# Optimization experiments

Hardware: AMD Instinct MI355X
Metric: run time of the kernel (lower is better)

Reference implementation:

```python
import jax, jax.numpy as jnp
import numpy as np

CTX_LEN = 7
TAU = 2.0      # curr_temp = max_temp at init
ALPHA = -1.0   # dist_to_logits_alpha


def _prelu(v, a):
    return jnp.where(v >= 0, v, a * v)


def setup_inputs() -> dict:
    key = jax.random.key(0)
    ks = jax.random.split(key, 8)
    B, T, D, M = 8, 4096, 256, 1024
    x = jax.random.normal(ks[0], (B, T, D), dtype=jnp.float32)
    noise = jax.random.normal(ks[1], (B, D, T - 1 + CTX_LEN), dtype=jnp.float32)
    gumbel_u = jax.random.uniform(ks[2], (B * T, M), dtype=jnp.float32)
    embedding = jax.random.uniform(ks[3], (1, M, D), dtype=jnp.float32)  # nn.init.uniform_
    w_ctx = jax.random.normal(ks[4], (D, D, CTX_LEN), dtype=jnp.float32) * 0.02
    w_f1 = jax.random.normal(ks[5], (D, 2 * D), dtype=jnp.float32) * 0.04
    w_f2 = jax.random.normal(ks[6], (D, 2 * D), dtype=jnp.float32) * 0.04
    a1 = jnp.array(0.5, dtype=jnp.float32)
    a2 = jnp.array(0.5, dtype=jnp.float32)
    return {"x": x, "noise": noise, "gumbel_u": gumbel_u, "epo": 10,
            "embedding": embedding, "w_ctx": w_ctx, "w_f1": w_f1, "a1": a1,
            "w_f2": w_f2, "a2": a2}


def reference(x, noise, gumbel_u, epo, embedding, w_ctx, w_f1, a1, w_f2, a2):
    B, T, D = x.shape
    E = embedding[0]                      # [M, D]
    M = E.shape[0]
    xt = jnp.transpose(x, (0, 2, 1))      # [B, D, T]
    # context input: x[:, :-1] permuted, left-padded by 1+7-1=7, detached
    ctx_in = jax.lax.stop_gradient(jnp.pad(xt[:, :, :T - 1], ((0, 0), (0, 0), (CTX_LEN, 0))))
    scale = jnp.sqrt(jnp.mean(ctx_in ** 2, axis=(1, 2), keepdims=True))
    ctx_in_noisy = jax.lax.stop_gradient(ctx_in + 0.5 * scale * noise * (0.5 ** (epo / 10.0)))
    ctx_out = jax.lax.conv_general_dilated(
        ctx_in_noisy, w_ctx, (1,), 'VALID',
        dimension_numbers=('NCH', 'OIH', 'NCH'))   # [B, D, T]
    # fuse 1 (1x1 conv == channel matmul) + PReLU
    cat1 = jnp.concatenate([xt, ctx_out], axis=1)            # [B, 2D, T]
    cur = _prelu(jnp.einsum('oc,bct->bot', w_f1, cat1), a1)  # [B, D, T]
    cur = jnp.transpose(cur, (0, 2, 1)).reshape(-1, D)       # [B*T, D]
    # squared distances via addmm equivalent, scaled to logits
    dist = (jnp.sum(cur ** 2, axis=1, keepdims=True)
            + jnp.sum(E ** 2, axis=1)
            - 2.0 * cur @ E.T)                               # [B*T, M]
    dm = ALPHA * dist
    # hard code usage entropy
    k = jnp.argmax(dm, axis=-1)
    hard_probs = jnp.mean(jax.nn.one_hot(k, M, dtype=dm.dtype), axis=0)
    code_perplexity = -jnp.sum(hard_probs * jnp.log2(hard_probs + 1e-10))
    # soft usage entropy
    avg_probs = jnp.mean(jax.nn.softmax(dm, axis=-1), axis=0)
    prob_perplexity = -jnp.sum(avg_probs * jnp.log2(avg_probs + 1e-10))
    # hard gumbel-softmax (straight-through)
    u = jnp.clip(gumbel_u, 1e-10, 1.0 - 1e-7)
    g = -jnp.log(-jnp.log(u))
    y_soft = jax.nn.softmax((dm + g) / TAU, axis=-1)
    idx = jnp.argmax(y_soft, axis=-1)
    y_hard = jax.nn.one_hot(idx, M, dtype=y_soft.dtype)
    dm_st = y_hard - jax.lax.stop_gradient(y_soft) + y_soft  # [B*T, M]
    quantization_inds = idx.reshape(B, T, 1)
    # dequantize: one-hot (straight-through) times codebook
    out_q = (dm_st @ E).reshape(B, T, D)
    # fuse 2 + PReLU
    cat2 = jnp.concatenate([jnp.transpose(out_q, (0, 2, 1)), ctx_out], axis=1)
    quantized = jnp.transpose(_prelu(jnp.einsum('oc,bct->bot', w_f2, cat2), a2), (0, 2, 1))
    return quantized, code_perplexity, prob_perplexity, quantization_inds
```

## Files before the change

### kernel.cpp

```cpp
#include <hip/hip_runtime.h>
#include <cmath>

#define B_    8
#define T_    4096
#define D_    256
#define M_    1024
#define L_    4102
#define LP_   4104
#define CTX_  7
#define NROW_ 32768

constexpr size_t OFF_DM    = 0;
constexpr size_t OFF_XT    = 0;
constexpr size_t OFF_CTXN  = 33554432;
constexpr size_t OFF_CURT  = 33554432;
constexpr size_t OFF_CTXO  = OFF_CTXN + (size_t)B_ * D_ * LP_;
constexpr size_t OFF_CUR2  = OFF_CTXO + (size_t)B_ * D_ * T_;
constexpr size_t OFF_SOFT  = OFF_CUR2 + NROW_;
constexpr size_t OFF_HIST  = OFF_SOFT + 4096;
constexpr size_t OFF_SUMSQ = OFF_HIST + 1024;
constexpr size_t OFF_ESQ   = OFF_SUMSQ + 16;
constexpr size_t OFF_IDX   = OFF_ESQ + 1024;
constexpr size_t OFF_ET    = OFF_IDX + NROW_;
constexpr size_t OFF_W1T   = OFF_ET + 262144;
constexpr size_t OFF_W2T   = OFF_W1T + 131072;
constexpr size_t OFF_WCT   = OFF_W2T + 131072;
constexpr size_t OFF_P     = OFF_WCT + 458752;

using s16x8 = __attribute__((ext_vector_type(8))) short;
using f32x4 = __attribute__((ext_vector_type(4))) float;

__device__ __forceinline__ ushort bf16rne(float f) {
  uint u = __float_as_uint(f);
  u += 0x7fffu + ((u >> 16) & 1u);
  return (ushort)(u >> 16);
}
__device__ __forceinline__ float bf16tof(ushort h) {
  return __uint_as_float((uint)h << 16);
}

__global__ __launch_bounds__(256) void k_prep(const float* __restrict__ emb,
                                              const float* __restrict__ wf1,
                                              const float* __restrict__ wf2,
                                              const float* __restrict__ wctx,
                                              const float* __restrict__ x,
                                              float* __restrict__ ET,
                                              float* __restrict__ W1T,
                                              float* __restrict__ W2T,
                                              ushort* __restrict__ WPF,
                                              float* __restrict__ esq,
                                              float* __restrict__ sumsq) {
  const int id = blockIdx.x;
  if (id < 512) {
    __shared__ float tile[32][33];
    const int tx = threadIdx.x & 31, ty = threadIdx.x >> 5;
    const float* src; float* dst; int R, C, c0, r0;
    if (id < 256)      { src = emb;  dst = ET;  R = 1024; C = 256;  c0 = (id & 7) << 5;  r0 = (id >> 3) << 5; }
    else if (id < 384) { const int r = id - 256; src = wf1; dst = W1T; R = 256; C = 512; c0 = (r & 15) << 5; r0 = (r >> 4) << 5; }
    else               { const int r = id - 384; src = wf2; dst = W2T; R = 256; C = 512; c0 = (r & 15) << 5; r0 = (r >> 4) << 5; }
    for (int rr = ty; rr < 32; rr += 8) {
      const int rI = r0 + rr, cI = c0 + tx;
      tile[rr][tx] = (rI < R && cI < C) ? src[(size_t)rI * C + cI] : 0.f;
    }
    __syncthreads();
    for (int rr = ty; rr < 32; rr += 8) {
      const int cI = c0 + rr, rI = r0 + tx;
      if (cI < C && rI < R) dst[(size_t)cI * R + rI] = tile[tx][rr];
    }
  } else if (id < 736) {
    const int K8 = id - 512;
    const int h = K8 >> 5, j = K8 & 31;
    const int o = threadIdx.x;
    uint hp[4], lp[4];
    #pragma unroll
    for (int e2 = 0; e2 < 4; ++e2) {
      ushort hs[2], ls[2];
      #pragma unroll
      for (int k = 0; k < 2; ++k) {
        const int i = (j << 3) + (e2 << 1) + k;
        const float v = wctx[(size_t)o * 1792 + (size_t)i * 7 + h];
        const ushort hb = bf16rne(v);
        hs[k] = hb;
        ls[k] = bf16rne(v - bf16tof(hb));
      }
      hp[e2] = (uint)hs[0] | ((uint)hs[1] << 16);
      lp[e2] = (uint)ls[0] | ((uint)ls[1] << 16);
    }
    uint4* W = (uint4*)WPF;
    W[(size_t)(K8 * 2) * 256 + o]     = make_uint4(hp[0], hp[1], hp[2], hp[3]);
    W[(size_t)(K8 * 2 + 1) * 256 + o] = make_uint4(lp[0], lp[1], lp[2], lp[3]);
  } else if (id < 992) {
    const int row = ((id - 736) << 2) + (threadIdx.x >> 6);
    const int lane = threadIdx.x & 63;
    const float4 v = ((const float4*)emb)[((size_t)row << 6) + lane];
    float s = v.x * v.x + v.y * v.y + v.z * v.z + v.w * v.w;
    #pragma unroll
    for (int off = 32; off; off >>= 1) s += __shfl_down(s, off, 64);
    if (lane == 0) esq[row] = s;
  } else {
    const int chunk = id - 992;
    const int b = chunk >> 6, sub = chunk & 63;
    const float4* xb = (const float4*)(x + (size_t)b * T_ * D_);
    const int N4 = (T_ - 1) * D_ / 4;
    float s = 0.f;
    for (int j = sub * 256 + threadIdx.x; j < N4; j += 64 * 256) {
      float4 v = xb[j];
      s += v.x * v.x + v.y * v.y + v.z * v.z + v.w * v.w;
    }
    #pragma unroll
    for (int off = 32; off; off >>= 1) s += __shfl_down(s, off, 64);
    __shared__ float red[4];
    const int lane = threadIdx.x & 63, wv = threadIdx.x >> 6;
    if (lane == 0) red[wv] = s;
    __syncthreads();
    if (threadIdx.x == 0) atomicAdd(&sumsq[b], (red[0] + red[1]) + (red[2] + red[3]));
  }
}

__global__ __launch_bounds__(256) void k_noisy(const float* __restrict__ x,
                                               const float* __restrict__ noise,
                                               const int* __restrict__ epo,
                                               const float* __restrict__ sumsq,
                                               ushort* __restrict__ inT,
                                               float* __restrict__ xT) {
  const int b = blockIdx.z;
  const int i0 = blockIdx.y << 5;
  const int tau0 = blockIdx.x << 5;
  const int tx = threadIdx.x & 31, ty = threadIdx.x >> 5;
  __shared__ float xt[32][33];
  __shared__ float nz[32][33];
  const int tr0 = tau0 - CTX_;
  for (int r = ty; r < 32; r += 8) {
    const int t = tr0 + r;
    xt[r][tx] = (t >= 0 && t < T_) ? x[((size_t)b * T_ + t) * D_ + i0 + tx] : 0.f;
  }
  for (int r = ty; r < 32; r += 8) {
    const int tau = tau0 + tx;
    nz[r][tx] = (tau < L_) ? noise[((size_t)b * D_ + i0 + r) * L_ + tau] : 0.f;
  }
  __syncthreads();
  const float scale = sqrtf(sumsq[b] * (1.0f / (256.0f * 4102.0f)));
  const float coef = 0.5f * powf(0.5f, (float)epo[0] * 0.1f) * scale;
  for (int r = ty; r < 32; r += 8) {
    const int i = i0 + r;
    const int tau = tau0 + tx;
    const float xv = xt[tx][r];
    if (tau >= CTX_ && tau < T_ + CTX_)
      xT[((size_t)b * D_ + i) * T_ + (tau - CTX_)] = xv;
  }
  if (threadIdx.x < 128) {
    const int tau_r = threadIdx.x >> 2, jl = threadIdx.x & 3;
    const int tau = tau0 + tau_r;
    if (tau < L_) {
      uint hp[4], lp[4];
      #pragma unroll
      for (int e2 = 0; e2 < 4; ++e2) {
        ushort hs[2], ls[2];
        #pragma unroll
        for (int k = 0; k < 2; ++k) {
          const int ir = (jl << 3) + (e2 << 1) + k;
          const float v = coef * nz[ir][tau_r] + xt[tau_r][ir];
          const ushort hb = bf16rne(v);
          hs[k] = hb;
          ls[k] = bf16rne(v - bf16tof(hb));
        }
        hp[e2] = (uint)hs[0] | ((uint)hs[1] << 16);
        lp[e2] = (uint)ls[0] | ((uint)ls[1] << 16);
      }
      const int j = (i0 >> 3) + jl;
      const int jsw = j ^ (tau & 7);
      ushort* dst = inT + ((size_t)b * LP_ + tau) * 256 + (jsw << 3);
      *(uint4*)dst = make_uint4(hp[0], hp[1], hp[2], hp[3]);
      *(uint4*)(dst + (size_t)B_ * LP_ * 256) = make_uint4(lp[0], lp[1], lp[2], lp[3]);
    }
  }
}

__global__ __launch_bounds__(256, 2) void k_convm(const ushort* __restrict__ WPF,
                                                  const ushort* __restrict__ inT,
                                                  float* __restrict__ ctxo) {
  const int t0 = blockIdx.x << 6;
  const int b  = blockIdx.y;
  const int tid = threadIdx.x;
  const int lane = tid & 63;
  const int wv = tid >> 6;
  const int ln = lane & 15, lg = lane >> 4;
  __shared__ ushort sB[2 * 72 * 256];
  {
    const size_t rb = ((size_t)b * LP_ + t0) * 256;
    const uint4* s4h = (const uint4*)(inT + rb);
    const uint4* s4l = (const uint4*)(inT + (size_t)B_ * LP_ * 256 + rb);
    uint4* d4 = (uint4*)sB;
    for (int q = tid; q < 2304; q += 256) d4[q] = s4h[q];
    for (int q = tid; q < 2304; q += 256) d4[2304 + q] = s4l[q];
  }
  __syncthreads();

  const f32x4 fz = {0.f, 0.f, 0.f, 0.f};
  f32x4 acc[4][4];
  #pragma unroll
  for (int i = 0; i < 4; ++i)
    #pragma unroll
    for (int j = 0; j < 4; ++j) acc[i][j] = fz;

  const ushort* wp = WPF + ((size_t)lg * 512 + (wv << 6) + ln) * 8;

  #pragma unroll 1
  for (int h = 0; h < 7; ++h) {
    #pragma unroll 1
    for (int js = 0; js < 8; ++js) {
      const int K8b = (h << 5) + (js << 2);
      s16x8 Af[2][4];
      #pragma unroll
      for (int to = 0; to < 4; ++to) {
        const ushort* ap = wp + (size_t)(K8b * 512 + (to << 4)) * 8;
        Af[0][to] = *(const s16x8*)ap;
        Af[1][to] = *(const s16x8*)(ap + 2048);
      }
      s16x8 Bf[2][4];
      #pragma unroll
      for (int tt = 0; tt < 4; ++tt) {
        const int r = (tt << 4) + ln + h;
        const int jsw = ((js << 2) + lg) ^ (r & 7);
        const int e0 = r * 256 + (jsw << 3);
        Bf[0][tt] = *(const s16x8*)&sB[e0];
        Bf[1][tt] = *(const s16x8*)&sB[18432 + e0];
      }
      #pragma unroll
      for (int to = 0; to < 4; ++to)
        #pragma unroll
        for (int tt = 0; tt < 4; ++tt) {
          acc[to][tt] = __builtin_amdgcn_mfma_f32_16x16x32_bf16(Af[0][to], Bf[0][tt], acc[to][tt], 0, 0, 0);
          acc[to][tt] = __builtin_amdgcn_mfma_f32_16x16x32_bf16(Af[0][to], Bf[1][tt], acc[to][tt], 0, 0, 0);
          acc[to][tt] = __builtin_amdgcn_mfma_f32_16x16x32_bf16(Af[1][to], Bf[0][tt], acc[to][tt], 0, 0, 0);
        }
    }
  }
  float* cb = ctxo + ((size_t)b * 256 + (wv << 6)) * T_ + t0;
  #pragma unroll
  for (int to = 0; to < 4; ++to)
    #pragma unroll
    for (int tt = 0; tt < 4; ++tt)
      #pragma unroll
      for (int rg = 0; rg < 4; ++rg) {
        const int o_loc = (to << 4) + (lg << 2) + rg;
        cb[(size_t)o_loc * T_ + (tt << 4) + ln] = acc[to][tt][rg];
      }
}

__device__ __forceinline__ void stage16x128(float* __restrict__ dst,
                                            const float* __restrict__ src,
                                            const int gstride, const int tid) {
  #pragma unroll
  for (int p = 0; p < 2; ++p) {
    const int q = p * 256 + tid;
    const int r = q >> 5, c = (q & 31) << 2;
    *(float4*)&dst[(r << 7) + c] = *(const float4*)&src[(size_t)r * gstride + c];
  }
}

__device__ __forceinline__ void gemm16s(const float* __restrict__ sA,
                                        const float* __restrict__ sB,
                                        const int ay, const int bx4,
                                        float acc[8][8]) {
  #pragma unroll 4
  for (int c = 0; c < 16; ++c) {
    const float4 a0 = *(const float4*)&sA[(c << 7) + ay];
    const float4 a1 = *(const float4*)&sA[(c << 7) + ay + 4];
    const float4 b0 = *(const float4*)&sB[(c << 7) + bx4];
    const float4 b1 = *(const float4*)&sB[(c << 7) + bx4 + 64];
    const float av[8] = {a0.x, a0.y, a0.z, a0.w, a1.x, a1.y, a1.z, a1.w};
    const float bv[8] = {b0.x, b0.y, b0.z, b0.w, b1.x, b1.y, b1.z, b1.w};
    #pragma unroll
    for (int i = 0; i < 8; ++i)
      #pragma unroll
      for (int j = 0; j < 8; ++j)
        acc[i][j] = fmaf(av[i], bv[j], acc[i][j]);
  }
}

__global__ __launch_bounds__(256) void k_fuse1(const float* __restrict__ xT,
                                               const float* __restrict__ ctxo,
                                               const float* __restrict__ w1T,
                                               const float* __restrict__ a1,
                                               float* __restrict__ curT,
                                               float* __restrict__ cur2) {
  const int bk = blockIdx.x;
  const int b = bk >> 5;
  const int t0 = (bk & 31) << 7;
  const int o0 = blockIdx.y << 7;
  const int tid = threadIdx.x;
  const int tx = tid & 15, ty = tid >> 4;
  const int ox = ty << 3, tp4 = tx << 2;
  __shared__ float smem[4096];
  float* sW = smem;
  float* sX = smem + 2048;
  float acc[8][8] = {};
  for (int cc = 0; cc < 512; cc += 16) {
    __syncthreads();
    stage16x128(sW, w1T + (size_t)cc * 256 + o0, 256, tid);
    const float* xsrc = (cc < 256)
        ? xT + ((size_t)b * D_ + cc) * T_ + t0
        : ctxo + ((size_t)b * D_ + (cc - 256)) * T_ + t0;
    stage16x128(sX, xsrc, T_, tid);
    __syncthreads();
    gemm16s(sW, sX, ox, tp4, acc);
  }
  const float alpha = a1[0];
  const size_t row0 = (size_t)b * T_ + t0;
  float part[8] = {};
  #pragma unroll
  for (int oo = 0; oo < 8; ++oo) {
    #pragma unroll
    for (int j = 0; j < 8; ++j) {
      float v = acc[oo][j];
      v = (v >= 0.f) ? v : alpha * v;
      acc[oo][j] = v;
      part[j] = fmaf(v, v, part[j]);
    }
    const float4 v0 = {acc[oo][0], acc[oo][1], acc[oo][2], acc[oo][3]};
    const float4 v1 = {acc[oo][4], acc[oo][5], acc[oo][6], acc[oo][7]};
    float* dst = curT + (size_t)(o0 + ox + oo) * NROW_ + row0;
    *(float4*)(dst + tp4) = v0;
    *(float4*)(dst + tp4 + 64) = v1;
  }
  __syncthreads();
  float* red = smem;
  #pragma unroll
  for (int j = 0; j < 4; ++j) {
    red[(tp4 + j) * 17 + ty] = part[j];
    red[(tp4 + 64 + j) * 17 + ty] = part[4 + j];
  }
  __syncthreads();
  if (tid < 128) {
    float s = 0.f;
    #pragma unroll
    for (int k = 0; k < 16; ++k) s += red[tid * 17 + k];
    atomicAdd(&cur2[row0 + tid], s);
  }
}

__global__ __launch_bounds__(256) void k_pmm(const float* __restrict__ ET,
                                             const float* __restrict__ w2T,
                                             float* __restrict__ P) {
  const int m0 = blockIdx.x << 7;
  const int o0 = blockIdx.y << 7;
  const int tid = threadIdx.x;
  const int tx = tid & 15, ty = tid >> 4;
  const int my = ty << 3, ox4 = tx << 2;
  __shared__ float smem[4096];
  float* sM = smem;
  float* sW = smem + 2048;
  float acc[8][8] = {};
  for (int cc = 0; cc < 256; cc += 16) {
    __syncthreads();
    stage16x128(sM, ET + (size_t)cc * M_ + m0, M_, tid);
    stage16x128(sW, w2T + (size_t)cc * 256 + o0, 256, tid);
    __syncthreads();
    gemm16s(sM, sW, my, ox4, acc);
  }
  #pragma unroll
  for (int mm = 0; mm < 8; ++mm) {
    const float4 v0 = {acc[mm][0], acc[mm][1], acc[mm][2], acc[mm][3]};
    const float4 v1 = {acc[mm][4], acc[mm][5], acc[mm][6], acc[mm][7]};
    float* dst = P + (size_t)(m0 + my + mm) * 256 + o0;
    *(float4*)(dst + ox4) = v0;
    *(float4*)(dst + ox4 + 64) = v1;
  }
}

__global__ __launch_bounds__(256) void k_dist(const float* __restrict__ curT,
                                              const float* __restrict__ ET,
                                              const float* __restrict__ cur2,
                                              const float* __restrict__ esq,
                                              float* __restrict__ dm) {
  const int r0 = blockIdx.x << 7;
  const int m0 = blockIdx.y << 7;
  const int tid = threadIdx.x;
  const int tx = tid & 15, ty = tid >> 4;
  const int ry = ty << 3, mx4 = tx << 2;
  __shared__ float smem[4096];
  float* sC = smem;
  float* sE = smem + 2048;
  float acc[8][8] = {};
  for (int cc = 0; cc < 256; cc += 16) {
    __syncthreads();
    stage16x128(sC, curT + (size_t)cc * NROW_ + r0, NROW_, tid);
    stage16x128(sE, ET + (size_t)cc * M_ + m0, M_, tid);
    __syncthreads();
    gemm16s(sC, sE, ry, mx4, acc);
  }
  float c2[8], eq0[4], eq1[4];
  *(float4*)&c2[0] = *(const float4*)&cur2[r0 + ry];
  *(float4*)&c2[4] = *(const float4*)&cur2[r0 + ry + 4];
  *(float4*)&eq0[0] = *(const float4*)&esq[m0 + mx4];
  *(float4*)&eq1[0] = *(const float4*)&esq[m0 + mx4 + 64];
  #pragma unroll
  for (int rr = 0; rr < 8; ++rr) {
    float o0v[4], o1v[4];
    #pragma unroll
    for (int j = 0; j < 4; ++j) {
      o0v[j] = -(c2[rr] + eq0[j] - 2.0f * acc[rr][j]);
      o1v[j] = -(c2[rr] + eq1[j] - 2.0f * acc[rr][j + 4]);
    }
    float* dst = dm + (size_t)(r0 + ry + rr) * M_ + m0;
    *(float4*)(dst + mx4) = *(float4*)&o0v[0];
    *(float4*)(dst + mx4 + 64) = *(float4*)&o1v[0];
  }
}

__global__ __launch_bounds__(256) void k_soft(const float* __restrict__ dm,
                                              const float* __restrict__ gu,
                                              float* __restrict__ soft4,
                                              unsigned* __restrict__ hist,
                                              int* __restrict__ idxi,
                                              float* __restrict__ idxf) {
  const int tid = threadIdx.x;
  const int lane = tid & 63, w = tid >> 6;
  __shared__ float accS[1024];
  __shared__ unsigned histS[1024];
  for (int j = tid; j < 1024; j += 256) { accS[j] = 0.f; histS[j] = 0u; }
  __syncthreads();
  float p[16] = {};
  const int rbase = (blockIdx.x << 6) + (w << 4);
  for (int rr = 0; rr < 16; ++rr) {
    const int r = rbase + rr;
    const float4* dr = (const float4*)(dm + ((size_t)r << 10));
    float v[16];
    #pragma unroll
    for (int k = 0; k < 4; ++k) {
      const float4 d = dr[lane + (k << 6)];
      v[k * 4 + 0] = d.x; v[k * 4 + 1] = d.y; v[k * 4 + 2] = d.z; v[k * 4 + 3] = d.w;
    }
    float mx = v[0];
    #pragma unroll
    for (int s = 1; s < 16; ++s) mx = fmaxf(mx, v[s]);
    #pragma unroll
    for (int m = 32; m; m >>= 1) mx = fmaxf(mx, __shfl_xor(mx, m, 64));
    float e[16]; float sum = 0.f;
    #pragma unroll
    for (int s = 0; s < 16; ++s) { e[s] = expf(v[s] - mx); sum += e[s]; }
    #pragma unroll
    for (int m = 32; m; m >>= 1) sum += __shfl_xor(sum, m, 64);
    const float inv = 1.0f / sum;
    #pragma unroll
    for (int s = 0; s < 16; ++s) p[s] = fmaf(e[s], inv, p[s]);
    float bv = v[0]; int bi = (lane << 2);
    #pragma unroll
    for (int s = 1; s < 16; ++s) {
      const int m_ = (lane << 2) + ((s >> 2) << 8) + (s & 3);
      if (v[s] > bv) { bv = v[s]; bi = m_; }
    }
    #pragma unroll
    for (int m = 32; m; m >>= 1) {
      const float ov = __shfl_xor(bv, m, 64);
      const int oi = __shfl_xor(bi, m, 64);
      if (ov > bv || (ov == bv && oi < bi)) { bv = ov; bi = oi; }
    }
    if (lane == 0) atomicAdd(&histS[bi], 1u);
    const float4* gr = (const float4*)(gu + ((size_t)r << 10));
    float z[16];
    #pragma unroll
    for (int k = 0; k < 4; ++k) {
      const float4 u = gr[lane + (k << 6)];
      const float uu[4] = {u.x, u.y, u.z, u.w};
      #pragma unroll
      for (int j = 0; j < 4; ++j) {
        const float uc = fminf(fmaxf(uu[j], 1e-10f), 1.0f - 1e-7f);
        z[k * 4 + j] = v[k * 4 + j] - logf(-logf(uc));
      }
    }
    bv = z[0]; bi = (lane << 2);
    #pragma unroll
    for (int s = 1; s < 16; ++s) {
      const int m_ = (lane << 2) + ((s >> 2) << 8) + (s & 3);
      if (z[s] > bv) { bv = z[s]; bi = m_; }
    }
    #pragma unroll
    for (int m = 32; m; m >>= 1) {
      const float ov = __shfl_xor(bv, m, 64);
      const int oi = __shfl_xor(bi, m, 64);
      if (ov > bv || (ov == bv && oi < bi)) { bv = ov; bi = oi; }
    }
    if (lane == 0) { idxi[r] = bi; idxf[r] = (float)bi; }
  }
  #pragma unroll
  for (int s = 0; s < 16; ++s)
    atomicAdd(&accS[(lane << 2) + ((s >> 2) << 8) + (s & 3)], p[s]);
  __syncthreads();
  const int rep = (blockIdx.x & 3) << 10;
  for (int j = tid; j < 1024; j += 256) {
    atomicAdd(&soft4[rep + j], accS[j]);
    const unsigned h = histS[j];
    if (h) atomicAdd(&hist[j], h);
  }
}

__global__ __launch_bounds__(256) void k_perp(const float* __restrict__ soft4,
                                              const unsigned* __restrict__ hist,
                                              float* __restrict__ out2) {
  const int tid = threadIdx.x;
  float cp = 0.f, pp = 0.f;
  for (int m = tid; m < 1024; m += 256) {
    const float hp = (float)hist[m] * (1.0f / 32768.0f);
    cp += hp * log2f(hp + 1e-10f);
    const float q = (soft4[m] + soft4[1024 + m] + soft4[2048 + m] + soft4[3072 + m]) * (1.0f / 32768.0f);
    pp += q * log2f(q + 1e-10f);
  }
  #pragma unroll
  for (int off = 32; off; off >>= 1) {
    cp += __shfl_down(cp, off, 64);
    pp += __shfl_down(pp, off, 64);
  }
  __shared__ float rc[4], rp[4];
  const int lane = tid & 63, wv = tid >> 6;
  if (lane == 0) { rc[wv] = cp; rp[wv] = pp; }
  __syncthreads();
  if (tid == 0) {
    out2[0] = -((rc[0] + rc[1]) + (rc[2] + rc[3]));
    out2[1] = -((rp[0] + rp[1]) + (rp[2] + rp[3]));
  }
}

__global__ __launch_bounds__(256) void k_fuse2m(const float* __restrict__ ctxo,
                                                const float* __restrict__ w2T,
                                                const float* __restrict__ P,
                                                const int* __restrict__ idxi,
                                                const float* __restrict__ a2,
                                                float* __restrict__ outq) {
  const int bk = blockIdx.x;
  const int b = bk >> 6;
  const int t0 = (bk & 63) << 6;
  const int tid = threadIdx.x;
  const int lane = tid & 63, wv = tid >> 6;
  const int ln = lane & 15, lg = lane >> 4;
  const int o0w = wv << 6;
  __shared__ int idxS[64];
  if (tid < 64) idxS[tid] = idxi[(size_t)b * T_ + t0 + tid];
  __syncthreads();

  const f32x4 fz = {0.f, 0.f, 0.f, 0.f};
  f32x4 acc[4][4];
  #pragma unroll
  for (int i = 0; i < 4; ++i)
    #pragma unroll
    for (int j = 0; j < 4; ++j) acc[i][j] = fz;

  #pragma unroll 1
  for (int ks = 0; ks < 8; ++ks) {
    const int cb = (ks << 5) + (lg << 3);
    s16x8 Af[4];
    #pragma unroll
    for (int to = 0; to < 4; ++to) {
      const float* wp = w2T + (size_t)(256 + cb) * 256 + o0w + (to << 4) + ln;
      #pragma unroll
      for (int e = 0; e < 8; ++e)
        Af[to][e] = (short)bf16rne(wp[(size_t)e * 256]);
    }
    s16x8 Bf[4];
    #pragma unroll
    for (int tt = 0; tt < 4; ++tt) {
      const float* xp = ctxo + ((size_t)b * D_ + cb) * T_ + t0 + (tt << 4) + ln;
      #pragma unroll
      for (int e = 0; e < 8; ++e)
        Bf[tt][e] = (short)bf16rne(xp[(size_t)e * T_]);
    }
    #pragma unroll
    for (int to = 0; to < 4; ++to)
      #pragma unroll
      for (int tt = 0; tt < 4; ++tt)
        acc[to][tt] = __builtin_amdgcn_mfma_f32_16x16x32_bf16(Af[to], Bf[tt], acc[to][tt], 0, 0, 0);
  }

  const float alpha = a2[0];
  #pragma unroll
  for (int tt = 0; tt < 4; ++tt) {
    const int t = t0 + (tt << 4) + ln;
    const int id = idxS[(tt << 4) + ln];
    #pragma unroll
    for (int to = 0; to < 4; ++to) {
      const int ob = o0w + (to << 4) + (lg << 2);
      const float4 p4 = *(const float4*)&P[(size_t)id * 256 + ob];
      const float pv[4] = {p4.x, p4.y, p4.z, p4.w};
      float o[4];
      #pragma unroll
      for (int rg = 0; rg < 4; ++rg) {
        const float v = acc[to][tt][rg] + pv[rg];
        o[rg] = (v >= 0.f) ? v : alpha * v;
      }
      *(float4*)&outq[((size_t)b * T_ + t) * D_ + ob] = *(float4*)&o[0];
    }
  }
}

extern "C" void kernel_launch(void* const* d_in, const int* in_sizes, int n_in,
                              void* d_out, int out_size, void* d_ws, size_t ws_size,
                              hipStream_t stream) {
  (void)in_sizes; (void)n_in; (void)out_size; (void)ws_size;
  const float* x     = (const float*)d_in[0];
  const float* noise = (const float*)d_in[1];
  const float* gu    = (const float*)d_in[2];
  const int*   epo   = (const int*)d_in[3];
  const float* emb   = (const float*)d_in[4];
  const float* wctx  = (const float*)d_in[5];
  const float* wf1   = (const float*)d_in[6];
  const float* a1    = (const float*)d_in[7];
  const float* wf2   = (const float*)d_in[8];
  const float* a2    = (const float*)d_in[9];

  float* ws    = (float*)d_ws;
  float* dm    = ws + OFF_DM;
  float* xT    = ws + OFF_XT;
  ushort* inT  = (ushort*)(ws + OFF_CTXN);
  float* curT  = ws + OFF_CURT;
  float* ctxo  = ws + OFF_CTXO;
  float* cur2  = ws + OFF_CUR2;
  float* soft  = ws + OFF_SOFT;
  unsigned* hist = (unsigned*)(ws + OFF_HIST);
  float* sumsq = ws + OFF_SUMSQ;
  float* esq   = ws + OFF_ESQ;
  int*   idxi  = (int*)(ws + OFF_IDX);
  float* ET    = ws + OFF_ET;
  float* W1T   = ws + OFF_W1T;
  float* W2T   = ws + OFF_W2T;
  ushort* WPF  = (ushort*)(ws + OFF_WCT);
  float* P     = ws + OFF_P;

  float* outq = (float*)d_out;
  float* scal = outq + (size_t)NROW_ * D_;
  float* idxf = scal + 2;

  hipMemsetAsync(ws + OFF_CUR2, 0, (NROW_ + 4096 + 1024 + 16) * sizeof(float), stream);

  k_prep  <<<1504, 256, 0, stream>>>(emb, wf1, wf2, wctx, x, ET, W1T, W2T, WPF, esq, sumsq);
  k_noisy <<<dim3(129, 8, 8), 256, 0, stream>>>(x, noise, epo, sumsq, inT, xT);
  k_convm <<<dim3(64, 8), 256, 0, stream>>>(WPF, inT, ctxo);
  k_fuse1 <<<dim3(256, 2), 256, 0, stream>>>(xT, ctxo, W1T, a1, curT, cur2);
  k_pmm   <<<dim3(8, 2), 256, 0, stream>>>(ET, W2T, P);
  k_dist  <<<dim3(256, 8), 256, 0, stream>>>(curT, ET, cur2, esq, dm);
  k_soft  <<<512, 256, 0, stream>>>(dm, gu, soft, hist, idxi, idxf);
  k_perp  <<<1, 256, 0, stream>>>(soft, hist, scal);
  k_fuse2m<<<512, 256, 0, stream>>>(ctxo, W2T, P, idxi, a2, outq);
}
```

Measured before the change: 790.0 us.

## Fuse distance GEMM with softmax/argmax epilogue to skip dm round-trip

Merges the distance GEMM and the softmax/gumbel/argmax kernel into one kernel. Each block computes a full 32x1024 row tile of logits in registers and reduces it directly, so the 128 MB dm matrix is never written to or read from global memory. In exchange, each block now stages the entire codebook slice (64 KB shared) per k-step, uses a less efficient 8x16 per-thread GEMM shape with a large register footprint, and rereads ET 1024 times.

```diff
diff --git a/kernel.cpp b/kernel.cpp
--- a/kernel.cpp
+++ b/kernel.cpp
@@ -10,7 +10,6 @@
 #define CTX_  7
 #define NROW_ 32768
 
-constexpr size_t OFF_DM    = 0;
 constexpr size_t OFF_XT    = 0;
 constexpr size_t OFF_CTXN  = 33554432;
 constexpr size_t OFF_CURT  = 33554432;
@@ -369,69 +368,74 @@
   }
 }
 
-__global__ __launch_bounds__(256) void k_dist(const float* __restrict__ curT,
-                                              const float* __restrict__ ET,
-                                              const float* __restrict__ cur2,
-                                              const float* __restrict__ esq,
-                                              float* __restrict__ dm) {
-  const int r0 = blockIdx.x << 7;
-  const int m0 = blockIdx.y << 7;
+__global__ __launch_bounds__(256, 2) void k_dsoft(const float* __restrict__ curT,
+                                                  const float* __restrict__ ET,
+                                                  const float* __restrict__ cur2,
+                                                  const float* __restrict__ esq,
+                                                  const float* __restrict__ gu,
+                                                  float* __restrict__ soft4,
+                                                  unsigned* __restrict__ hist,
+                                                  int* __restrict__ idxi,
+                                                  float* __restrict__ idxf) {
   const int tid = threadIdx.x;
-  const int tx = tid & 15, ty = tid >> 4;
-  const int ry = ty << 3, mx4 = tx << 2;
-  __shared__ float smem[4096];
-  float* sC = smem;
-  float* sE = smem + 2048;
-  float acc[8][8] = {};
-  for (int cc = 0; cc < 256; cc += 16) {
-    __syncthreads();
-    stage16x128(sC, curT + (size_t)cc * NROW_ + r0, NROW_, tid);
-    stage16x128(sE, ET + (size_t)cc * M_ + m0, M_, tid);
-    __syncthreads();
-    gemm16s(sC, sE, ry, mx4, acc);
-  }
-  float c2[8], eq0[4], eq1[4];
-  *(float4*)&c2[0] = *(const float4*)&cur2[r0 + ry];
-  *(float4*)&c2[4] = *(const float4*)&cur2[r0 + ry + 4];
-  *(float4*)&eq0[0] = *(const float4*)&esq[m0 + mx4];
-  *(float4*)&eq1[0] = *(const float4*)&esq[m0 + mx4 + 64];
-  #pragma unroll
-  for (int rr = 0; rr < 8; ++rr) {
-    float o0v[4], o1v[4];
-    #pragma unroll
-    for (int j = 0; j < 4; ++j) {
-      o0v[j] = -(c2[rr] + eq0[j] - 2.0f * acc[rr][j]);
-      o1v[j] = -(c2[rr] + eq1[j] - 2.0f * acc[rr][j + 4]);
-    }
-    float* dst = dm + (size_t)(r0 + ry + rr) * M_ + m0;
-    *(float4*)(dst + mx4) = *(float4*)&o0v[0];
-    *(float4*)(dst + mx4 + 64) = *(float4*)&o1v[0];
-  }
-}
-
-__global__ __launch_bounds__(256) void k_soft(const float* __restrict__ dm,
-                                              const float* __restrict__ gu,
-                                              float* __restrict__ soft4,
-                                              unsigned* __restrict__ hist,
-                                              int* __restrict__ idxi,
-                                              float* __restrict__ idxf) {
-  const int tid = threadIdx.x;
-  const int lane = tid & 63, w = tid >> 6;
+  const int lane = tid & 63, wv = tid >> 6;
+  const int r0 = blockIdx.x << 5;
+  __shared__ float sC[16 * 32];
+  __shared__ float sE[16 * 1024];
   __shared__ float accS[1024];
   __shared__ unsigned histS[1024];
   for (int j = tid; j < 1024; j += 256) { accS[j] = 0.f; histS[j] = 0u; }
-  __syncthreads();
+
+  float acc[8][16];
+  #pragma unroll
+  for (int rr = 0; rr < 8; ++rr)
+    #pragma unroll
+    for (int s = 0; s < 16; ++s) acc[rr][s] = 0.f;
+
+  for (int cc = 0; cc < 256; cc += 16) {
+    __syncthreads();
+    if (tid < 128) {
+      const int c = tid >> 3, o = (tid & 7) << 2;
+      *(float4*)&sC[c * 32 + o] = *(const float4*)&curT[(size_t)(cc + c) * NROW_ + r0 + o];
+    }
+    #pragma unroll
+    for (int p = 0; p < 16; ++p) {
+      const int q = p * 256 + tid;
+      const int c = q >> 8, m = (q & 255) << 2;
+      *(float4*)&sE[c * 1024 + m] = *(const float4*)&ET[(size_t)(cc + c) * M_ + m];
+    }
+    __syncthreads();
+    #pragma unroll 4
+    for (int c = 0; c < 16; ++c) {
+      float a[8];
+      *(float4*)&a[0] = *(const float4*)&sC[c * 32 + (wv << 3)];
+      *(float4*)&a[4] = *(const float4*)&sC[c * 32 + (wv << 3) + 4];
+      float bb[16];
+      #pragma unroll
+      for (int q = 0; q < 4; ++q)
+        *(float4*)&bb[q << 2] = *(const float4*)&sE[c * 1024 + (q << 8) + (lane << 2)];
+      #pragma unroll
+      for (int rr = 0; rr < 8; ++rr)
+        #pragma unroll
+        for (int s = 0; s < 16; ++s)
+          acc[rr][s] = fmaf(a[rr], bb[s], acc[rr][s]);
+    }
+  }
+
+  float e2v[16];
+  #pragma unroll
+  for (int q = 0; q < 4; ++q)
+    *(float4*)&e2v[q << 2] = *(const float4*)&esq[(q << 8) + (lane << 2)];
+
   float p[16] = {};
-  const int rbase = (blockIdx.x << 6) + (w << 4);
-  for (int rr = 0; rr < 16; ++rr) {
+  const int rbase = r0 + (wv << 3);
+  for (int rr = 0; rr < 8; ++rr) {
     const int r = rbase + rr;
-    const float4* dr = (const float4*)(dm + ((size_t)r << 10));
+    const float c2r = cur2[r];
     float v[16];
     #pragma unroll
-    for (int k = 0; k < 4; ++k) {
-      const float4 d = dr[lane + (k << 6)];
-      v[k * 4 + 0] = d.x; v[k * 4 + 1] = d.y; v[k * 4 + 2] = d.z; v[k * 4 + 3] = d.w;
-    }
+    for (int s = 0; s < 16; ++s)
+      v[s] = -(c2r + e2v[s] - 2.0f * acc[rr][s]);
     float mx = v[0];
     #pragma unroll
     for (int s = 1; s < 16; ++s) mx = fmaxf(mx, v[s]);
@@ -609,7 +613,6 @@
   const float* a2    = (const float*)d_in[9];
 
   float* ws    = (float*)d_ws;
-  float* dm    = ws + OFF_DM;
   float* xT    = ws + OFF_XT;
   ushort* inT  = (ushort*)(ws + OFF_CTXN);
   float* curT  = ws + OFF_CURT;
@@ -637,8 +640,7 @@
   k_convm <<<dim3(64, 8), 256, 0, stream>>>(WPF, inT, ctxo);
   k_fuse1 <<<dim3(256, 2), 256, 0, stream>>>(xT, ctxo, W1T, a1, curT, cur2);
   k_pmm   <<<dim3(8, 2), 256, 0, stream>>>(ET, W2T, P);
-  k_dist  <<<dim3(256, 8), 256, 0, stream>>>(curT, ET, cur2, esq, dm);
-  k_soft  <<<512, 256, 0, stream>>>(dm, gu, soft, hist, idxi, idxf);
+  k_dsoft <<<1024, 256, 0, stream>>>(curT, ET, cur2, esq, gu, soft, hist, idxi, idxf);
   k_perp  <<<1, 256, 0, stream>>>(soft, hist, scal);
   k_fuse2m<<<512, 256, 0, stream>>>(ctxo, W2T, P, idxi, a2, outq);
 }
```

New measurement: 1.027 ms. +30.0%, slower.
